# Kernel tuning notes

Measured on AMD Instinct MI355X. Metric: run time of the kernel, lower is better.

The kernel has to match this reference:

```python
import jax, jax.numpy as jnp
import numpy as np
import math

LS = [0, 1, 2]            # degrees present in all irreps
MAX_L = 2
MULT_IN = 64
MULT_MID = 16
MULT_OUT = 64
N = 20000

# ---- Clebsch-Gordan coefficients in the real spherical-harmonic basis ----

def _f(n):
    return math.factorial(int(n))

def _cg_complex(j1, m1, j2, m2, j3, m3):
    if m1 + m2 != m3:
        return 0.0
    pre = math.sqrt((2 * j3 + 1) * _f(j1 + j2 - j3) * _f(j1 - j2 + j3) * _f(-j1 + j2 + j3) / _f(j1 + j2 + j3 + 1))
    pre *= math.sqrt(_f(j1 + m1) * _f(j1 - m1) * _f(j2 + m2) * _f(j2 - m2) * _f(j3 + m3) * _f(j3 - m3))
    kmin = max(0, j2 - j3 - m1, j1 - j3 + m2)
    kmax = min(j1 + j2 - j3, j1 - m1, j2 + m2)
    s = 0.0
    for k in range(kmin, kmax + 1):
        s += (-1) ** k / (_f(k) * _f(j1 + j2 - j3 - k) * _f(j1 - m1 - k) * _f(j2 + m2 - k) * _f(j3 - j2 + m1 + k) * _f(j3 - j1 - m2 + k))
    return pre * s

def _q(l):
    # complex->real change of basis, rows indexed by real m = -l..l
    Q = np.zeros((2 * l + 1, 2 * l + 1), dtype=complex)
    Q[l, l] = 1.0
    r2 = math.sqrt(2.0)
    for m in range(1, l + 1):
        Q[l + m, l + m] = (-1) ** m / r2
        Q[l + m, l - m] = 1.0 / r2
        Q[l - m, l - m] = 1j / r2
        Q[l - m, l + m] = -1j * (-1) ** m / r2
    return Q

def _real_cg(l1, l2, l3):
    C = np.zeros((2 * l1 + 1, 2 * l2 + 1, 2 * l3 + 1), dtype=complex)
    for m1 in range(-l1, l1 + 1):
        for m2 in range(-l2, l2 + 1):
            m3 = m1 + m2
            if -l3 <= m3 <= l3:
                C[l1 + m1, l2 + m2, l3 + m3] = _cg_complex(l1, m1, l2, m2, l3, m3)
    Q1, Q2, Q3 = _q(l1), _q(l2), _q(l3)
    M = np.einsum('ia,jb,kc,abc->ijk', Q1.conj(), Q2.conj(), Q3, C)
    if np.abs(M.imag).max() > np.abs(M.real).max():
        M = M * (-1j)  # fix parity phase so coefficients are real
    assert np.abs(M.imag).max() < 1e-10
    return np.asarray(M.real, dtype=np.float32)

# triangle-rule paths, truncated at MAX_L
PATHS = [(l1, l2, l) for l1 in LS for l2 in LS for l in range(abs(l1 - l2), min(l1 + l2, MAX_L) + 1)]
CG = {p: jnp.asarray(_real_cg(*p)) for p in PATHS}


def setup_inputs() -> dict:
    key = jax.random.key(0)
    ks = jax.random.split(key, 12)
    inp = {}
    for i, l in enumerate(LS):
        inp[f'x{l}'] = jax.random.normal(ks[i], (N, MULT_IN, 2 * l + 1), dtype=jnp.float32)
    for i, l in enumerate(LS):
        inp[f'W1_{l}'] = jax.random.normal(ks[3 + i], (MULT_IN, MULT_MID), dtype=jnp.float32)
        inp[f'W2_{l}'] = jax.random.normal(ks[6 + i], (MULT_IN, MULT_MID), dtype=jnp.float32)
    tp_mults = {l: sum(MULT_MID * MULT_MID for (l1, l2, lo) in PATHS if lo == l) for l in LS}
    for i, l in enumerate(LS):
        inp[f'W3_{l}'] = jax.random.normal(ks[9 + i], (tp_mults[l], MULT_OUT), dtype=jnp.float32)
    return inp


def _linear(x, W):
    # x: [n, u, i], W: [u, v] -> [n, v, i], normalized like e3nn Linear
    return jnp.einsum('nui,uv->nvi', x, W) / np.float32(math.sqrt(x.shape[1]))


def reference(x0, x1, x2, W1_0, W1_1, W1_2, W2_0, W2_1, W2_2, W3_0, W3_1, W3_2):
    xs = [x0, x1, x2]
    W1 = [W1_0, W1_1, W1_2]
    W2 = [W2_0, W2_1, W2_2]
    W3 = [W3_0, W3_1, W3_2]
    a = [_linear(xs[l], W1[l]) for l in LS]   # branch 1
    b = [_linear(xs[l], W2[l]) for l in LS]   # branch 2
    # CG tensor product up to MAX_L, full (uv) multiplicity
    tp = {l: [] for l in LS}
    n = x0.shape[0]
    for (l1, l2, l) in PATHS:
        t = jnp.einsum('nui,nvj,ijk->nuvk', a[l1], b[l2], CG[(l1, l2, l)])
        tp[l].append(t.reshape(n, MULT_MID * MULT_MID, 2 * l + 1))
    outs = []
    for l in LS:
        z = jnp.concatenate(tp[l], axis=1)        # [n, tp_mult_l, 2l+1]
        y = _linear(z, W3[l])                     # [n, MULT_OUT, 2l+1]
        outs.append(y.reshape(n, -1))
    return jnp.concatenate(outs, axis=1)          # [n, MULT_OUT * 9]
```

## Files before the change

kernel.cpp:

```cpp
#include <hip/hip_runtime.h>


typedef __attribute__((ext_vector_type(4))) float f32x4;
typedef __attribute__((ext_vector_type(4))) float f4;
typedef __attribute__((ext_vector_type(2))) float f2;
typedef __attribute__((ext_vector_type(8))) short short8;
typedef unsigned short ushort_t;
typedef unsigned int uint32;

__device__ __forceinline__ uint32 bfb(float x) {
  uint32 u = __float_as_uint(x);
  return (u + 0x7fffu + ((u >> 16) & 1u)) >> 16;
}
__device__ __forceinline__ uint32 pack2f(f2 z) {
  uint32 lo = __float_as_uint(z.x) + 0x8000u;
  uint32 hi = __float_as_uint(z.y) + 0x8000u;
  return __builtin_amdgcn_perm(hi, lo, 0x07060302u);
}

#define C2   0.7071067811865476f
#define C3   0.5773502691896258f
#define C5   0.4472135954999579f
#define C6   0.4082482904638631f
#define C23  0.8164965809277260f
#define C10  0.3162277660168379f
#define C210 0.6324555320336759f
#define C310 0.5477225575051661f
#define C14  0.2672612419124244f
#define C214 0.5345224838248488f
#define C314 0.4629100498862757f

__global__ __launch_bounds__(256) void pack_w3_kernel(
    const float* __restrict__ W30, const float* __restrict__ W31,
    const float* __restrict__ W32, ushort_t* __restrict__ pack) {
  int lc = blockIdx.x;
  int t = threadIdx.x >> 6;
  int lam = threadIdx.x & 63;
  const float* W;
  int mb;
  float nrm;
  if (lc < 24) {
    W = W30; mb = lc * 32; nrm = 0.036084391824351615f;
  } else if (lc < 72) {
    W = W31; mb = (lc - 24) * 32; nrm = 0.025515518153991442f;
  } else {
    W = W32; mb = (lc - 72) * 32; nrm = 0.025515518153991442f;
  }
  int w = t * 16 + (lam & 15);
  int m0 = mb + (lam >> 4) * 8;
  ushort_t* dst = pack + ((size_t)(lc * 4 + t) * 64 + lam) * 8;
#pragma unroll
  for (int j = 0; j < 8; ++j)
    dst[j] = (ushort_t)bfb(W[(size_t)(m0 + j) * 64 + w] * nrm);
}

template <int NK, int JD, class F>
__device__ __forceinline__ void zgenv(const float* bsj, ushort_t* zrow, F f) {
  uint32 zp[NK][8];
#pragma unroll
  for (int oc = 0; oc < 2; ++oc) {
    f2 bb4[JD][4];
#pragma unroll
    for (int j = 0; j < JD; ++j) {
      f4 lo = *(const f4*)(bsj + j * 16 + oc * 8);
      f4 hi = *(const f4*)(bsj + j * 16 + oc * 8 + 4);
      bb4[j][0] = lo.xy; bb4[j][1] = lo.zw;
      bb4[j][2] = hi.xy; bb4[j][3] = hi.zw;
    }
#pragma unroll
    for (int q = 0; q < 4; ++q) {
      f2 bcol[JD], z[NK];
#pragma unroll
      for (int j = 0; j < JD; ++j) bcol[j] = bb4[j][q];
      f(bcol, z);
#pragma unroll
      for (int k = 0; k < NK; ++k) zp[k][oc * 4 + q] = pack2f(z[k]);
    }
  }
#pragma unroll
  for (int k = 0; k < NK; ++k) {
    uint32* d = (uint32*)(zrow + k * (16 * 264));
    *(uint4*)(d) = make_uint4(zp[k][0], zp[k][1], zp[k][2], zp[k][3]);
    *(uint4*)(d + 4) = make_uint4(zp[k][4], zp[k][5], zp[k][6], zp[k][7]);
  }
}

template <int NROW>
__device__ __forceinline__ void mfma2(const ushort_t* zb, const ushort_t* pk,
                                      int pcbase, int h, int wt0, int lane,
                                      f32x4* accA, f32x4* accB) {
  const int srow = lane & 15, quad = lane >> 4;
  const ushort_t* ab = zb + srow * 264 + quad * 8 + h * 128;
  const ushort_t* bb = pk + ((size_t)((pcbase + h * 4) * 4 + wt0) * 64 + lane) * 8;
#pragma unroll
  for (int c = 0; c < 4; ++c) {
    short8 B0 = *(const short8*)(bb + (size_t)c * 2048);
    short8 B1 = *(const short8*)(bb + (size_t)c * 2048 + 512);
#pragma unroll
    for (int rt = 0; rt < NROW; ++rt) {
      short8 A = *(const short8*)(ab + rt * (16 * 264) + c * 32);
      accA[rt] = __builtin_amdgcn_mfma_f32_16x16x32_bf16(A, B0, accA[rt], 0, 0, 0);
      accB[rt] = __builtin_amdgcn_mfma_f32_16x16x32_bf16(A, B1, accB[rt], 0, 0, 0);
    }
  }
}

#define ZB 12672

__global__ __launch_bounds__(256, 2) void tdense_kernel(
    const float* __restrict__ x0, const float* __restrict__ x1,
    const float* __restrict__ x2, const float* __restrict__ W10,
    const float* __restrict__ W20, const float* __restrict__ W11,
    const float* __restrict__ W21, const float* __restrict__ W12,
    const float* __restrict__ W22, const ushort_t* __restrict__ pack,
    float* __restrict__ out) {
  __shared__ float b_s[2368];
  __shared__ __align__(16) ushort_t zbuf[2 * ZB];

  const int tid = threadIdx.x;
  const int nbase = blockIdx.x * 16;
  const int s = tid >> 4, v = tid & 15;

  const int n = nbase + s;
  const float* px0 = x0 + (size_t)n * 64;
  const float* px1 = x1 + (size_t)n * 192;
  const float* px2 = x2 + (size_t)n * 320;
  float a0 = 0.f, a1x = 0.f, a1y = 0.f, a1z = 0.f;
  float a2[5] = {0.f, 0.f, 0.f, 0.f, 0.f};
  float b0 = 0.f, b1x = 0.f, b1y = 0.f, b1z = 0.f;
  float b2[5] = {0.f, 0.f, 0.f, 0.f, 0.f};
  for (int u4 = 0; u4 < 16; ++u4) {
    f4 xv0 = *(const f4*)(px0 + u4 * 4);
    f4 xa = *(const f4*)(px1 + u4 * 12);
    f4 xb = *(const f4*)(px1 + u4 * 12 + 4);
    f4 xc = *(const f4*)(px1 + u4 * 12 + 8);
    f4 ya = *(const f4*)(px2 + u4 * 20);
    f4 yb = *(const f4*)(px2 + u4 * 20 + 4);
    f4 yc = *(const f4*)(px2 + u4 * 20 + 8);
    f4 yd = *(const f4*)(px2 + u4 * 20 + 12);
    f4 ye = *(const f4*)(px2 + u4 * 20 + 16);
    float x1e[12], x2e[20];
#pragma unroll
    for (int e = 0; e < 4; ++e) { x1e[e] = xa[e]; x1e[4 + e] = xb[e]; x1e[8 + e] = xc[e]; }
#pragma unroll
    for (int e = 0; e < 4; ++e) {
      x2e[e] = ya[e]; x2e[4 + e] = yb[e]; x2e[8 + e] = yc[e];
      x2e[12 + e] = yd[e]; x2e[16 + e] = ye[e];
    }
#pragma unroll
    for (int r = 0; r < 4; ++r) {
      int u = u4 * 4 + r;
      float wa0 = W10[u * 16 + v], wb0 = W20[u * 16 + v];
      float wa1 = W11[u * 16 + v], wb1 = W21[u * 16 + v];
      float wa2 = W12[u * 16 + v], wb2 = W22[u * 16 + v];
      float xx = xv0[r];
      a0 += xx * wa0; b0 += xx * wb0;
      float e0 = x1e[r * 3 + 0], e1 = x1e[r * 3 + 1], e2 = x1e[r * 3 + 2];
      a1x += e0 * wa1; a1y += e1 * wa1; a1z += e2 * wa1;
      b1x += e0 * wb1; b1y += e1 * wb1; b1z += e2 * wb1;
#pragma unroll
      for (int j = 0; j < 5; ++j) {
        float ev = x2e[r * 5 + j];
        a2[j] += ev * wa2;
        b2[j] += ev * wb2;
      }
    }
  }
  const float inv8 = 0.125f;
  float ar[9];
  ar[0] = a0 * inv8;
  ar[1] = a1x * inv8; ar[2] = a1y * inv8; ar[3] = a1z * inv8;
#pragma unroll
  for (int j = 0; j < 5; ++j) ar[4 + j] = a2[j] * inv8;
  {
    float* bw = b_s + s * 148 + v;
    bw[0] = b0 * inv8;
    bw[16] = b1x * inv8; bw[32] = b1y * inv8; bw[48] = b1z * inv8;
#pragma unroll
    for (int j = 0; j < 5; ++j) bw[64 + j * 16] = b2[j] * inv8;
  }

  const int lane = tid & 63;
  const int wv = tid >> 6;
  const int p2 = (wv & 1) * 2;
  const int h = wv >> 1;

  f32x4 aA0, aB0, aA1[3], aB1[3], aA2[5], aB2[5];
  aA0 = (f32x4)(0.f); aB0 = (f32x4)(0.f);
#pragma unroll
  for (int i = 0; i < 3; ++i) { aA1[i] = (f32x4)(0.f); aB1[i] = (f32x4)(0.f); }
#pragma unroll
  for (int i = 0; i < 5; ++i) { aA2[i] = (f32x4)(0.f); aB2[i] = (f32x4)(0.f); }

  const float* bsl0 = b_s + s * 148;
  const float* bsl1 = bsl0 + 16;
  const float* bsl2 = bsl0 + 64;
  ushort_t* z0 = zbuf + s * 264 + v * 16;
  ushort_t* z1 = z0 + ZB;
  const ushort_t* Zb0 = zbuf;
  const ushort_t* Zb1 = zbuf + ZB;

  zgenv<1, 1>(bsl0, z0, [&](const f2* b, f2* z) { z[0] = ar[0] * b[0]; });
  zgenv<1, 3>(bsl1, z0 + 4224, [&](const f2* b, f2* z) {
    z[0] = -C3 * (ar[1] * b[0] + ar[2] * b[1] + ar[3] * b[2]);
  });
  zgenv<1, 5>(bsl2, z0 + 8448, [&](const f2* b, f2* z) {
    z[0] = C5 * (ar[4] * b[0] + ar[5] * b[1] + ar[6] * b[2] + ar[7] * b[3] + ar[8] * b[4]);
  });
  __syncthreads();

  zgenv<3, 3>(bsl1, z1, [&](const f2* b, f2* z) {
    z[0] = ar[0] * b[0]; z[1] = ar[0] * b[1]; z[2] = ar[0] * b[2];
  });
  mfma2<1>(Zb0, pack, 0, h, p2, lane, &aA0, &aB0);
  mfma2<1>(Zb0 + 4224, pack, 8, h, p2, lane, &aA0, &aB0);
  mfma2<1>(Zb0 + 8448, pack, 16, h, p2, lane, &aA0, &aB0);
  __syncthreads();

  zgenv<3, 1>(bsl0, z0, [&](const f2* b, f2* z) {
    z[0] = ar[1] * b[0]; z[1] = ar[2] * b[0]; z[2] = ar[3] * b[0];
  });
  mfma2<3>(Zb1, pack, 24, h, p2, lane, aA1, aB1);
  __syncthreads();

  zgenv<3, 3>(bsl1, z1, [&](const f2* b, f2* z) {
    z[0] = C2 * (ar[2] * b[2] - ar[3] * b[1]);
    z[1] = C2 * (ar[3] * b[0] - ar[1] * b[2]);
    z[2] = C2 * (ar[1] * b[1] - ar[2] * b[0]);
  });
  mfma2<3>(Zb0, pack, 32, h, p2, lane, aA1, aB1);
  __syncthreads();

  zgenv<3, 5>(bsl2, z0, [&](const f2* b, f2* z) {
    z[0] = -C310 * ar[2] * b[1] + C10 * ar[1] * b[2] - C310 * ar[3] * b[0] + C310 * ar[1] * b[4];
    z[1] = -C210 * ar[2] * b[2] - C310 * ar[3] * b[3] - C310 * ar[1] * b[1];
    z[2] = -C310 * ar[2] * b[3] + C10 * ar[3] * b[2] - C310 * ar[1] * b[0] - C310 * ar[3] * b[4];
  });
  mfma2<3>(Zb1, pack, 40, h, p2, lane, aA1, aB1);
  __syncthreads();

  zgenv<3, 3>(bsl1, z1, [&](const f2* b, f2* z) {
    z[0] = -C310 * ar[5] * b[1] + C10 * ar[6] * b[0] - C310 * ar[4] * b[2] + C310 * ar[8] * b[0];
    z[1] = -C210 * ar[6] * b[1] - C310 * ar[7] * b[2] - C310 * ar[5] * b[0];
    z[2] = -C310 * ar[7] * b[1] + C10 * ar[6] * b[2] - C310 * ar[4] * b[0] - C310 * ar[8] * b[2];
  });
  mfma2<3>(Zb0, pack, 48, h, p2, lane, aA1, aB1);
  __syncthreads();

  zgenv<3, 5>(bsl2, z0, [&](const f2* b, f2* z) {
    z[0] = C10 * (ar[8] * b[3] - ar[7] * b[4] + ar[4] * b[1] - ar[5] * b[0]) +
           C310 * (ar[7] * b[2] - ar[6] * b[3]);
    z[1] = C10 * (ar[5] * b[3] - ar[7] * b[1]) + C210 * (ar[4] * b[4] - ar[8] * b[0]);
    z[2] = C10 * (ar[8] * b[1] - ar[5] * b[4] + ar[7] * b[0] - ar[4] * b[3]) +
           C310 * (ar[6] * b[1] - ar[5] * b[2]);
  });
  mfma2<3>(Zb1, pack, 56, h, p2, lane, aA1, aB1);
  __syncthreads();

  zgenv<3, 5>(bsl2, z1, [&](const f2* b, f2* z) {
    z[0] = ar[0] * b[0]; z[1] = ar[0] * b[1]; z[2] = ar[0] * b[2];
  });
  mfma2<3>(Zb0, pack, 64, h, p2, lane, aA1, aB1);
  __syncthreads();

  zgenv<2, 5>(bsl2, z0, [&](const f2* b, f2* z) {
    z[0] = ar[0] * b[3]; z[1] = ar[0] * b[4];
  });
  mfma2<3>(Zb1, pack, 72, h, p2, lane, aA2, aB2);
  __syncthreads();

  zgenv<3, 3>(bsl1, z1, [&](const f2* b, f2* z) {
    z[0] = C2 * (ar[1] * b[2] + ar[3] * b[0]);
    z[1] = C2 * (ar[2] * b[0] + ar[1] * b[1]);
    z[2] = C23 * ar[2] * b[1] - C6 * (ar[1] * b[0] + ar[3] * b[2]);
  });
  mfma2<2>(Zb0, pack, 72, h, p2, lane, aA2 + 3, aB2 + 3);
  __syncthreads();

  zgenv<2, 3>(bsl1, z0, [&](const f2* b, f2* z) {
    z[0] = C2 * (ar[2] * b[2] + ar[3] * b[1]);
    z[1] = C2 * (ar[3] * b[2] - ar[1] * b[0]);
  });
  mfma2<3>(Zb1, pack, 80, h, p2, lane, aA2, aB2);
  __syncthreads();

  zgenv<3, 5>(bsl2, z1, [&](const f2* b, f2* z) {
    z[0] = C23 * ar[2] * b[4] + C6 * ar[1] * b[1] - C6 * ar[3] * b[3];
    z[1] = C6 * ar[2] * b[3] - C6 * ar[1] * b[0] - C2 * ar[3] * b[2] - C6 * ar[3] * b[4];
    z[2] = C2 * (ar[3] * b[1] - ar[1] * b[3]);
  });
  mfma2<2>(Zb0, pack, 80, h, p2, lane, aA2 + 3, aB2 + 3);
  __syncthreads();

  zgenv<2, 5>(bsl2, z0, [&](const f2* b, f2* z) {
    z[0] = -C6 * ar[2] * b[1] + C2 * ar[1] * b[2] + C6 * ar[3] * b[0] - C6 * ar[1] * b[4];
    z[1] = -C23 * ar[2] * b[0] + C6 * ar[1] * b[3] + C6 * ar[3] * b[1];
  });
  mfma2<3>(Zb1, pack, 88, h, p2, lane, aA2, aB2);
  __syncthreads();

  zgenv<3, 1>(bsl0, z1, [&](const f2* b, f2* z) {
    z[0] = ar[4] * b[0]; z[1] = ar[5] * b[0]; z[2] = ar[6] * b[0];
  });
  mfma2<2>(Zb0, pack, 88, h, p2, lane, aA2 + 3, aB2 + 3);
  __syncthreads();

  zgenv<2, 1>(bsl0, z0, [&](const f2* b, f2* z) {
    z[0] = ar[7] * b[0]; z[1] = ar[8] * b[0];
  });
  mfma2<3>(Zb1, pack, 96, h, p2, lane, aA2, aB2);
  __syncthreads();

  zgenv<3, 3>(bsl1, z1, [&](const f2* b, f2* z) {
    z[0] = -C23 * ar[8] * b[1] - C6 * ar[5] * b[0] + C6 * ar[7] * b[2];
    z[1] = -C6 * ar[7] * b[1] + C6 * ar[4] * b[0] + C2 * ar[6] * b[2] + C6 * ar[8] * b[2];
    z[2] = C2 * (ar[7] * b[0] - ar[5] * b[2]);
  });
  mfma2<2>(Zb0, pack, 96, h, p2, lane, aA2 + 3, aB2 + 3);
  __syncthreads();

  zgenv<2, 3>(bsl1, z0, [&](const f2* b, f2* z) {
    z[0] = C6 * ar[5] * b[1] - C2 * ar[6] * b[0] - C6 * ar[4] * b[2] + C6 * ar[8] * b[0];
    z[1] = C23 * ar[4] * b[1] - C6 * ar[7] * b[0] - C6 * ar[5] * b[2];
  });
  mfma2<3>(Zb1, pack, 104, h, p2, lane, aA2, aB2);
  __syncthreads();

  zgenv<3, 5>(bsl2, z1, [&](const f2* b, f2* z) {
    z[0] = C214 * (ar[6] * b[0] + ar[4] * b[2]) - C314 * (ar[5] * b[3] + ar[7] * b[1]);
    z[1] = -C14 * (ar[6] * b[1] + ar[5] * b[2]) + C314 * (ar[5] * b[4] + ar[8] * b[1]) -
           C314 * (ar[7] * b[0] + ar[4] * b[3]);
    z[2] = -C214 * ar[6] * b[2] - C14 * (ar[5] * b[1] + ar[7] * b[3]) +
           C214 * (ar[4] * b[0] + ar[8] * b[4]);
  });
  mfma2<2>(Zb0, pack, 104, h, p2, lane, aA2 + 3, aB2 + 3);
  __syncthreads();

  zgenv<2, 5>(bsl2, z0, [&](const f2* b, f2* z) {
    z[0] = -C14 * (ar[6] * b[3] + ar[7] * b[2]) - C314 * (ar[5] * b[0] + ar[4] * b[1]) -
           C314 * (ar[7] * b[4] + ar[8] * b[3]);
    z[1] = C214 * (ar[6] * b[4] + ar[8] * b[2]) + C314 * (ar[5] * b[1] - ar[7] * b[3]);
  });
  mfma2<3>(Zb1, pack, 112, h, p2, lane, aA2, aB2);
  __syncthreads();

  mfma2<2>(Zb0, pack, 112, h, p2, lane, aA2 + 3, aB2 + 3);
  __syncthreads();

  float* red = (float*)zbuf;
  const int col = lane & 15, quad = lane >> 4;
  if (h == 0) {
#pragma unroll
    for (int pp = 0; pp < 2; ++pp) {
      int wt = p2 + pp;
      const f32x4* src0 = pp ? &aB0 : &aA0;
      const f32x4* src1 = pp ? aB1 : aA1;
      const f32x4* src2 = pp ? aB2 : aA2;
      *(f4*)(red + (wt * 9 + 0) * 256 + lane * 4) = src0[0];
#pragma unroll
      for (int o = 0; o < 3; ++o)
        *(f4*)(red + (wt * 9 + 1 + o) * 256 + lane * 4) = src1[o];
#pragma unroll
      for (int o = 0; o < 5; ++o)
        *(f4*)(red + (wt * 9 + 4 + o) * 256 + lane * 4) = src2[o];
    }
  }
  __syncthreads();
  if (h == 1) {
    aA0 += *(const f4*)(red + (p2 * 9 + 0) * 256 + lane * 4);
    aB0 += *(const f4*)(red + ((p2 + 1) * 9 + 0) * 256 + lane * 4);
#pragma unroll
    for (int o = 0; o < 3; ++o) {
      aA1[o] += *(const f4*)(red + (p2 * 9 + 1 + o) * 256 + lane * 4);
      aB1[o] += *(const f4*)(red + ((p2 + 1) * 9 + 1 + o) * 256 + lane * 4);
    }
#pragma unroll
    for (int o = 0; o < 5; ++o) {
      aA2[o] += *(const f4*)(red + (p2 * 9 + 4 + o) * 256 + lane * 4);
      aB2[o] += *(const f4*)(red + ((p2 + 1) * 9 + 4 + o) * 256 + lane * 4);
    }
    const int w0 = p2 * 16 + col, w1 = w0 + 16;
#pragma unroll
    for (int r = 0; r < 4; ++r) {
      int so = quad * 4 + r;
      float* row = out + (size_t)(nbase + so) * 576;
      row[w0] = aA0[r];
      row[w1] = aB0[r];
      row[64 + w0 * 3 + 0] = aA1[0][r];
      row[64 + w0 * 3 + 1] = aA1[1][r];
      row[64 + w0 * 3 + 2] = aA1[2][r];
      row[64 + w1 * 3 + 0] = aB1[0][r];
      row[64 + w1 * 3 + 1] = aB1[1][r];
      row[64 + w1 * 3 + 2] = aB1[2][r];
#pragma unroll
      for (int k = 0; k < 5; ++k) {
        row[256 + w0 * 5 + k] = aA2[k][r];
        row[256 + w1 * 5 + k] = aB2[k][r];
      }
    }
  }
}

extern "C" void kernel_launch(void* const* d_in, const int* in_sizes, int n_in,
                              void* d_out, int out_size, void* d_ws, size_t ws_size,
                              hipStream_t stream) {
  const float* x0 = (const float*)d_in[0];
  const float* x1 = (const float*)d_in[1];
  const float* x2 = (const float*)d_in[2];
  const float* W10 = (const float*)d_in[3];
  const float* W20 = (const float*)d_in[4];
  const float* W11 = (const float*)d_in[5];
  const float* W21 = (const float*)d_in[6];
  const float* W12 = (const float*)d_in[7];
  const float* W22 = (const float*)d_in[8];
  const float* W30 = (const float*)d_in[9];
  const float* W31 = (const float*)d_in[10];
  const float* W32 = (const float*)d_in[11];
  ushort_t* pack = (ushort_t*)d_ws;

  hipLaunchKernelGGL(pack_w3_kernel, dim3(120), dim3(256), 0, stream,
                     W30, W31, W32, pack);

  int nsamp = in_sizes[0] / 64;
  int nblocks = nsamp / 16;
  hipLaunchKernelGGL(tdense_kernel, dim3(nblocks), dim3(256), 0, stream,
                     x0, x1, x2, W10, W20, W11, W21, W12, W22, pack,
                     (float*)d_out);
}
```

Baseline: 220.2 us.

## Collapse tensor-product dense kernel to one wavefront per 16-sample block

Each 16-sample block now runs on a single 64-lane wavefront instead of four waves. Every lane computes four mid-channels, loading the first-linear weights as vectors, and one wave runs the full K and N range of the MFMA output linear. This removes the cross-wave split-K reduction through LDS and most of the inter-wave barriers. In exchange each wave carries more registers and serial work, and latency hiding must come from more resident blocks, since launch bounds now allow one 64-thread block.

Result: slower. 590.2 us (+168.1%).

```diff
diff --git a/kernel.cpp b/kernel.cpp
--- a/kernel.cpp
+++ b/kernel.cpp
@@ -68,13 +68,13 @@
       bb4[j][2] = hi.xy; bb4[j][3] = hi.zw;
     }
 #pragma unroll
-    for (int q = 0; q < 4; ++q) {
+    for (int qp = 0; qp < 4; ++qp) {
       f2 bcol[JD], z[NK];
 #pragma unroll
-      for (int j = 0; j < JD; ++j) bcol[j] = bb4[j][q];
+      for (int j = 0; j < JD; ++j) bcol[j] = bb4[j][qp];
       f(bcol, z);
 #pragma unroll
-      for (int k = 0; k < NK; ++k) zp[k][oc * 4 + q] = pack2f(z[k]);
+      for (int k = 0; k < NK; ++k) zp[k][oc * 4 + qp] = pack2f(z[k]);
     }
   }
 #pragma unroll
@@ -85,50 +85,54 @@
   }
 }
 
-template <int NROW>
-__device__ __forceinline__ void mfma2(const ushort_t* zb, const ushort_t* pk,
-                                      int pcbase, int h, int wt0, int lane,
-                                      f32x4* accA, f32x4* accB) {
+template <int NROW, int NC, int M0>
+__device__ __forceinline__ void mfma_full(const ushort_t* zb,
+                                          const ushort_t* pkl, int pcbase,
+                                          int lane, f32x4 (&acc)[4][NC]) {
   const int srow = lane & 15, quad = lane >> 4;
-  const ushort_t* ab = zb + srow * 264 + quad * 8 + h * 128;
-  const ushort_t* bb = pk + ((size_t)((pcbase + h * 4) * 4 + wt0) * 64 + lane) * 8;
-#pragma unroll
-  for (int c = 0; c < 4; ++c) {
-    short8 B0 = *(const short8*)(bb + (size_t)c * 2048);
-    short8 B1 = *(const short8*)(bb + (size_t)c * 2048 + 512);
+  const ushort_t* ab = zb + srow * 264 + quad * 8;
+#pragma unroll
+  for (int c = 0; c < 8; ++c) {
+    const ushort_t* bb = pkl + (size_t)(pcbase + c) * 2048;
+    short8 B0 = *(const short8*)(bb);
+    short8 B1 = *(const short8*)(bb + 512);
+    short8 B2 = *(const short8*)(bb + 1024);
+    short8 B3 = *(const short8*)(bb + 1536);
 #pragma unroll
     for (int rt = 0; rt < NROW; ++rt) {
-      short8 A = *(const short8*)(ab + rt * (16 * 264) + c * 32);
-      accA[rt] = __builtin_amdgcn_mfma_f32_16x16x32_bf16(A, B0, accA[rt], 0, 0, 0);
-      accB[rt] = __builtin_amdgcn_mfma_f32_16x16x32_bf16(A, B1, accB[rt], 0, 0, 0);
-    }
-  }
-}
-
-#define ZB 12672
-
-__global__ __launch_bounds__(256, 2) void tdense_kernel(
+      short8 A = *(const short8*)(ab + rt * 4224 + c * 32);
+      acc[0][M0 + rt] = __builtin_amdgcn_mfma_f32_16x16x32_bf16(A, B0, acc[0][M0 + rt], 0, 0, 0);
+      acc[1][M0 + rt] = __builtin_amdgcn_mfma_f32_16x16x32_bf16(A, B1, acc[1][M0 + rt], 0, 0, 0);
+      acc[2][M0 + rt] = __builtin_amdgcn_mfma_f32_16x16x32_bf16(A, B2, acc[2][M0 + rt], 0, 0, 0);
+      acc[3][M0 + rt] = __builtin_amdgcn_mfma_f32_16x16x32_bf16(A, B3, acc[3][M0 + rt], 0, 0, 0);
+    }
+  }
+}
+
+__global__ __launch_bounds__(64, 1) void tdense_kernel(
     const float* __restrict__ x0, const float* __restrict__ x1,
     const float* __restrict__ x2, const float* __restrict__ W10,
     const float* __restrict__ W20, const float* __restrict__ W11,
     const float* __restrict__ W21, const float* __restrict__ W12,
     const float* __restrict__ W22, const ushort_t* __restrict__ pack,
     float* __restrict__ out) {
-  __shared__ float b_s[2368];
-  __shared__ __align__(16) ushort_t zbuf[2 * ZB];
-
-  const int tid = threadIdx.x;
+  __shared__ __align__(16) float lds_b[16 * 148];
+  __shared__ __align__(16) ushort_t zls[3 * 16 * 264];
+
+  const int lane = threadIdx.x;
+  const int s = lane & 15, q = lane >> 4;
   const int nbase = blockIdx.x * 16;
-  const int s = tid >> 4, v = tid & 15;
-
   const int n = nbase + s;
+
   const float* px0 = x0 + (size_t)n * 64;
   const float* px1 = x1 + (size_t)n * 192;
   const float* px2 = x2 + (size_t)n * 320;
-  float a0 = 0.f, a1x = 0.f, a1y = 0.f, a1z = 0.f;
-  float a2[5] = {0.f, 0.f, 0.f, 0.f, 0.f};
-  float b0 = 0.f, b1x = 0.f, b1y = 0.f, b1z = 0.f;
-  float b2[5] = {0.f, 0.f, 0.f, 0.f, 0.f};
+  float av_[4][9], bv_[4][9];
+#pragma unroll
+  for (int vi = 0; vi < 4; ++vi)
+#pragma unroll
+    for (int i = 0; i < 9; ++i) { av_[vi][i] = 0.f; bv_[vi][i] = 0.f; }
+  const int wq = q * 4;
   for (int u4 = 0; u4 < 16; ++u4) {
     f4 xv0 = *(const f4*)(px0 + u4 * 4);
     f4 xa = *(const f4*)(px1 + u4 * 12);
@@ -150,252 +154,341 @@
 #pragma unroll
     for (int r = 0; r < 4; ++r) {
       int u = u4 * 4 + r;
-      float wa0 = W10[u * 16 + v], wb0 = W20[u * 16 + v];
-      float wa1 = W11[u * 16 + v], wb1 = W21[u * 16 + v];
-      float wa2 = W12[u * 16 + v], wb2 = W22[u * 16 + v];
+      f4 wa0 = *(const f4*)(W10 + u * 16 + wq);
+      f4 wb0 = *(const f4*)(W20 + u * 16 + wq);
+      f4 wa1 = *(const f4*)(W11 + u * 16 + wq);
+      f4 wb1 = *(const f4*)(W21 + u * 16 + wq);
+      f4 wa2 = *(const f4*)(W12 + u * 16 + wq);
+      f4 wb2 = *(const f4*)(W22 + u * 16 + wq);
       float xx = xv0[r];
-      a0 += xx * wa0; b0 += xx * wb0;
-      float e0 = x1e[r * 3 + 0], e1 = x1e[r * 3 + 1], e2 = x1e[r * 3 + 2];
-      a1x += e0 * wa1; a1y += e1 * wa1; a1z += e2 * wa1;
-      b1x += e0 * wb1; b1y += e1 * wb1; b1z += e2 * wb1;
-#pragma unroll
-      for (int j = 0; j < 5; ++j) {
-        float ev = x2e[r * 5 + j];
-        a2[j] += ev * wa2;
-        b2[j] += ev * wb2;
+      float e0 = x1e[r * 3], e1 = x1e[r * 3 + 1], e2 = x1e[r * 3 + 2];
+#pragma unroll
+      for (int vi = 0; vi < 4; ++vi) {
+        av_[vi][0] += xx * wa0[vi]; bv_[vi][0] += xx * wb0[vi];
+        av_[vi][1] += e0 * wa1[vi]; av_[vi][2] += e1 * wa1[vi]; av_[vi][3] += e2 * wa1[vi];
+        bv_[vi][1] += e0 * wb1[vi]; bv_[vi][2] += e1 * wb1[vi]; bv_[vi][3] += e2 * wb1[vi];
+#pragma unroll
+        for (int jj = 0; jj < 5; ++jj) {
+          float ev = x2e[r * 5 + jj];
+          av_[vi][4 + jj] += ev * wa2[vi];
+          bv_[vi][4 + jj] += ev * wb2[vi];
+        }
       }
     }
   }
+
   const float inv8 = 0.125f;
-  float ar[9];
-  ar[0] = a0 * inv8;
-  ar[1] = a1x * inv8; ar[2] = a1y * inv8; ar[3] = a1z * inv8;
-#pragma unroll
-  for (int j = 0; j < 5; ++j) ar[4 + j] = a2[j] * inv8;
-  {
-    float* bw = b_s + s * 148 + v;
-    bw[0] = b0 * inv8;
-    bw[16] = b1x * inv8; bw[32] = b1y * inv8; bw[48] = b1z * inv8;
-#pragma unroll
-    for (int j = 0; j < 5; ++j) bw[64 + j * 16] = b2[j] * inv8;
-  }
-
-  const int lane = tid & 63;
-  const int wv = tid >> 6;
-  const int p2 = (wv & 1) * 2;
-  const int h = wv >> 1;
-
-  f32x4 aA0, aB0, aA1[3], aB1[3], aA2[5], aB2[5];
-  aA0 = (f32x4)(0.f); aB0 = (f32x4)(0.f);
-#pragma unroll
-  for (int i = 0; i < 3; ++i) { aA1[i] = (f32x4)(0.f); aB1[i] = (f32x4)(0.f); }
-#pragma unroll
-  for (int i = 0; i < 5; ++i) { aA2[i] = (f32x4)(0.f); aB2[i] = (f32x4)(0.f); }
-
-  const float* bsl0 = b_s + s * 148;
+#pragma unroll
+  for (int vi = 0; vi < 4; ++vi)
+#pragma unroll
+    for (int i = 0; i < 9; ++i) av_[vi][i] *= inv8;
+#pragma unroll
+  for (int j = 0; j < 9; ++j) {
+    f4 bw = {bv_[0][j], bv_[1][j], bv_[2][j], bv_[3][j]};
+    *(f4*)(lds_b + s * 148 + j * 16 + q * 4) = bw * inv8;
+  }
+  __syncthreads();
+
+  const float* bsl0 = lds_b + s * 148;
   const float* bsl1 = bsl0 + 16;
   const float* bsl2 = bsl0 + 64;
-  ushort_t* z0 = zbuf + s * 264 + v * 16;
-  ushort_t* z1 = z0 + ZB;
-  const ushort_t* Zb0 = zbuf;
-  const ushort_t* Zb1 = zbuf + ZB;
-
-  zgenv<1, 1>(bsl0, z0, [&](const f2* b, f2* z) { z[0] = ar[0] * b[0]; });
-  zgenv<1, 3>(bsl1, z0 + 4224, [&](const f2* b, f2* z) {
-    z[0] = -C3 * (ar[1] * b[0] + ar[2] * b[1] + ar[3] * b[2]);
-  });
-  zgenv<1, 5>(bsl2, z0 + 8448, [&](const f2* b, f2* z) {
-    z[0] = C5 * (ar[4] * b[0] + ar[5] * b[1] + ar[6] * b[2] + ar[7] * b[3] + ar[8] * b[4]);
-  });
-  __syncthreads();
-
-  zgenv<3, 3>(bsl1, z1, [&](const f2* b, f2* z) {
-    z[0] = ar[0] * b[0]; z[1] = ar[0] * b[1]; z[2] = ar[0] * b[2];
-  });
-  mfma2<1>(Zb0, pack, 0, h, p2, lane, &aA0, &aB0);
-  mfma2<1>(Zb0 + 4224, pack, 8, h, p2, lane, &aA0, &aB0);
-  mfma2<1>(Zb0 + 8448, pack, 16, h, p2, lane, &aA0, &aB0);
-  __syncthreads();
-
-  zgenv<3, 1>(bsl0, z0, [&](const f2* b, f2* z) {
-    z[0] = ar[1] * b[0]; z[1] = ar[2] * b[0]; z[2] = ar[3] * b[0];
-  });
-  mfma2<3>(Zb1, pack, 24, h, p2, lane, aA1, aB1);
-  __syncthreads();
-
-  zgenv<3, 3>(bsl1, z1, [&](const f2* b, f2* z) {
-    z[0] = C2 * (ar[2] * b[2] - ar[3] * b[1]);
-    z[1] = C2 * (ar[3] * b[0] - ar[1] * b[2]);
-    z[2] = C2 * (ar[1] * b[1] - ar[2] * b[0]);
-  });
-  mfma2<3>(Zb0, pack, 32, h, p2, lane, aA1, aB1);
-  __syncthreads();
-
-  zgenv<3, 5>(bsl2, z0, [&](const f2* b, f2* z) {
-    z[0] = -C310 * ar[2] * b[1] + C10 * ar[1] * b[2] - C310 * ar[3] * b[0] + C310 * ar[1] * b[4];
-    z[1] = -C210 * ar[2] * b[2] - C310 * ar[3] * b[3] - C310 * ar[1] * b[1];
-    z[2] = -C310 * ar[2] * b[3] + C10 * ar[3] * b[2] - C310 * ar[1] * b[0] - C310 * ar[3] * b[4];
-  });
-  mfma2<3>(Zb1, pack, 40, h, p2, lane, aA1, aB1);
-  __syncthreads();
-
-  zgenv<3, 3>(bsl1, z1, [&](const f2* b, f2* z) {
-    z[0] = -C310 * ar[5] * b[1] + C10 * ar[6] * b[0] - C310 * ar[4] * b[2] + C310 * ar[8] * b[0];
-    z[1] = -C210 * ar[6] * b[1] - C310 * ar[7] * b[2] - C310 * ar[5] * b[0];
-    z[2] = -C310 * ar[7] * b[1] + C10 * ar[6] * b[2] - C310 * ar[4] * b[0] - C310 * ar[8] * b[2];
-  });
-  mfma2<3>(Zb0, pack, 48, h, p2, lane, aA1, aB1);
-  __syncthreads();
-
-  zgenv<3, 5>(bsl2, z0, [&](const f2* b, f2* z) {
-    z[0] = C10 * (ar[8] * b[3] - ar[7] * b[4] + ar[4] * b[1] - ar[5] * b[0]) +
-           C310 * (ar[7] * b[2] - ar[6] * b[3]);
-    z[1] = C10 * (ar[5] * b[3] - ar[7] * b[1]) + C210 * (ar[4] * b[4] - ar[8] * b[0]);
-    z[2] = C10 * (ar[8] * b[1] - ar[5] * b[4] + ar[7] * b[0] - ar[4] * b[3]) +
-           C310 * (ar[6] * b[1] - ar[5] * b[2]);
-  });
-  mfma2<3>(Zb1, pack, 56, h, p2, lane, aA1, aB1);
-  __syncthreads();
-
-  zgenv<3, 5>(bsl2, z1, [&](const f2* b, f2* z) {
-    z[0] = ar[0] * b[0]; z[1] = ar[0] * b[1]; z[2] = ar[0] * b[2];
-  });
-  mfma2<3>(Zb0, pack, 64, h, p2, lane, aA1, aB1);
-  __syncthreads();
-
-  zgenv<2, 5>(bsl2, z0, [&](const f2* b, f2* z) {
-    z[0] = ar[0] * b[3]; z[1] = ar[0] * b[4];
-  });
-  mfma2<3>(Zb1, pack, 72, h, p2, lane, aA2, aB2);
-  __syncthreads();
-
-  zgenv<3, 3>(bsl1, z1, [&](const f2* b, f2* z) {
-    z[0] = C2 * (ar[1] * b[2] + ar[3] * b[0]);
-    z[1] = C2 * (ar[2] * b[0] + ar[1] * b[1]);
-    z[2] = C23 * ar[2] * b[1] - C6 * (ar[1] * b[0] + ar[3] * b[2]);
-  });
-  mfma2<2>(Zb0, pack, 72, h, p2, lane, aA2 + 3, aB2 + 3);
-  __syncthreads();
-
-  zgenv<2, 3>(bsl1, z0, [&](const f2* b, f2* z) {
-    z[0] = C2 * (ar[2] * b[2] + ar[3] * b[1]);
-    z[1] = C2 * (ar[3] * b[2] - ar[1] * b[0]);
-  });
-  mfma2<3>(Zb1, pack, 80, h, p2, lane, aA2, aB2);
-  __syncthreads();
-
-  zgenv<3, 5>(bsl2, z1, [&](const f2* b, f2* z) {
-    z[0] = C23 * ar[2] * b[4] + C6 * ar[1] * b[1] - C6 * ar[3] * b[3];
-    z[1] = C6 * ar[2] * b[3] - C6 * ar[1] * b[0] - C2 * ar[3] * b[2] - C6 * ar[3] * b[4];
-    z[2] = C2 * (ar[3] * b[1] - ar[1] * b[3]);
-  });
-  mfma2<2>(Zb0, pack, 80, h, p2, lane, aA2 + 3, aB2 + 3);
-  __syncthreads();
-
-  zgenv<2, 5>(bsl2, z0, [&](const f2* b, f2* z) {
-    z[0] = -C6 * ar[2] * b[1] + C2 * ar[1] * b[2] + C6 * ar[3] * b[0] - C6 * ar[1] * b[4];
-    z[1] = -C23 * ar[2] * b[0] + C6 * ar[1] * b[3] + C6 * ar[3] * b[1];
-  });
-  mfma2<3>(Zb1, pack, 88, h, p2, lane, aA2, aB2);
-  __syncthreads();
-
-  zgenv<3, 1>(bsl0, z1, [&](const f2* b, f2* z) {
-    z[0] = ar[4] * b[0]; z[1] = ar[5] * b[0]; z[2] = ar[6] * b[0];
-  });
-  mfma2<2>(Zb0, pack, 88, h, p2, lane, aA2 + 3, aB2 + 3);
-  __syncthreads();
-
-  zgenv<2, 1>(bsl0, z0, [&](const f2* b, f2* z) {
-    z[0] = ar[7] * b[0]; z[1] = ar[8] * b[0];
-  });
-  mfma2<3>(Zb1, pack, 96, h, p2, lane, aA2, aB2);
-  __syncthreads();
-
-  zgenv<3, 3>(bsl1, z1, [&](const f2* b, f2* z) {
-    z[0] = -C23 * ar[8] * b[1] - C6 * ar[5] * b[0] + C6 * ar[7] * b[2];
-    z[1] = -C6 * ar[7] * b[1] + C6 * ar[4] * b[0] + C2 * ar[6] * b[2] + C6 * ar[8] * b[2];
-    z[2] = C2 * (ar[7] * b[0] - ar[5] * b[2]);
-  });
-  mfma2<2>(Zb0, pack, 96, h, p2, lane, aA2 + 3, aB2 + 3);
-  __syncthreads();
-
-  zgenv<2, 3>(bsl1, z0, [&](const f2* b, f2* z) {
-    z[0] = C6 * ar[5] * b[1] - C2 * ar[6] * b[0] - C6 * ar[4] * b[2] + C6 * ar[8] * b[0];
-    z[1] = C23 * ar[4] * b[1] - C6 * ar[7] * b[0] - C6 * ar[5] * b[2];
-  });
-  mfma2<3>(Zb1, pack, 104, h, p2, lane, aA2, aB2);
-  __syncthreads();
-
-  zgenv<3, 5>(bsl2, z1, [&](const f2* b, f2* z) {
-    z[0] = C214 * (ar[6] * b[0] + ar[4] * b[2]) - C314 * (ar[5] * b[3] + ar[7] * b[1]);
-    z[1] = -C14 * (ar[6] * b[1] + ar[5] * b[2]) + C314 * (ar[5] * b[4] + ar[8] * b[1]) -
-           C314 * (ar[7] * b[0] + ar[4] * b[3]);
-    z[2] = -C214 * ar[6] * b[2] - C14 * (ar[5] * b[1] + ar[7] * b[3]) +
-           C214 * (ar[4] * b[0] + ar[8] * b[4]);
-  });
-  mfma2<2>(Zb0, pack, 104, h, p2, lane, aA2 + 3, aB2 + 3);
-  __syncthreads();
-
-  zgenv<2, 5>(bsl2, z0, [&](const f2* b, f2* z) {
-    z[0] = -C14 * (ar[6] * b[3] + ar[7] * b[2]) - C314 * (ar[5] * b[0] + ar[4] * b[1]) -
-           C314 * (ar[7] * b[4] + ar[8] * b[3]);
-    z[1] = C214 * (ar[6] * b[4] + ar[8] * b[2]) + C314 * (ar[5] * b[1] - ar[7] * b[3]);
-  });
-  mfma2<3>(Zb1, pack, 112, h, p2, lane, aA2, aB2);
-  __syncthreads();
-
-  mfma2<2>(Zb0, pack, 112, h, p2, lane, aA2 + 3, aB2 + 3);
-  __syncthreads();
-
-  float* red = (float*)zbuf;
-  const int col = lane & 15, quad = lane >> 4;
-  if (h == 0) {
-#pragma unroll
-    for (int pp = 0; pp < 2; ++pp) {
-      int wt = p2 + pp;
-      const f32x4* src0 = pp ? &aB0 : &aA0;
-      const f32x4* src1 = pp ? aB1 : aA1;
-      const f32x4* src2 = pp ? aB2 : aA2;
-      *(f4*)(red + (wt * 9 + 0) * 256 + lane * 4) = src0[0];
-#pragma unroll
-      for (int o = 0; o < 3; ++o)
-        *(f4*)(red + (wt * 9 + 1 + o) * 256 + lane * 4) = src1[o];
-#pragma unroll
-      for (int o = 0; o < 5; ++o)
-        *(f4*)(red + (wt * 9 + 4 + o) * 256 + lane * 4) = src2[o];
-    }
-  }
-  __syncthreads();
-  if (h == 1) {
-    aA0 += *(const f4*)(red + (p2 * 9 + 0) * 256 + lane * 4);
-    aB0 += *(const f4*)(red + ((p2 + 1) * 9 + 0) * 256 + lane * 4);
-#pragma unroll
-    for (int o = 0; o < 3; ++o) {
-      aA1[o] += *(const f4*)(red + (p2 * 9 + 1 + o) * 256 + lane * 4);
-      aB1[o] += *(const f4*)(red + ((p2 + 1) * 9 + 1 + o) * 256 + lane * 4);
-    }
-#pragma unroll
-    for (int o = 0; o < 5; ++o) {
-      aA2[o] += *(const f4*)(red + (p2 * 9 + 4 + o) * 256 + lane * 4);
-      aB2[o] += *(const f4*)(red + ((p2 + 1) * 9 + 4 + o) * 256 + lane * 4);
-    }
-    const int w0 = p2 * 16 + col, w1 = w0 + 16;
+  const ushort_t* pkl = pack + (size_t)lane * 8;
+  ushort_t* zr = zls + s * 264 + (q * 4) * 16;
+  const int ncol = s, rq4 = q * 4;
+
+  {
+    f32x4 acc[4][1];
+#pragma unroll
+    for (int wt = 0; wt < 4; ++wt) acc[wt][0] = (f32x4)(0.f);
+#pragma unroll
+    for (int vi = 0; vi < 4; ++vi) {
+      const float* arp = av_[vi];
+      ushort_t* zv = zr + vi * 16;
+      zgenv<1, 1>(bsl0, zv, [&](const f2* b, f2* z) { z[0] = arp[0] * b[0]; });
+      zgenv<1, 3>(bsl1, zv + 4224, [&](const f2* b, f2* z) {
+        z[0] = -C3 * (arp[1] * b[0] + arp[2] * b[1] + arp[3] * b[2]);
+      });
+      zgenv<1, 5>(bsl2, zv + 8448, [&](const f2* b, f2* z) {
+        z[0] = C5 * (arp[4] * b[0] + arp[5] * b[1] + arp[6] * b[2] +
+                     arp[7] * b[3] + arp[8] * b[4]);
+      });
+    }
+    __syncthreads();
+    mfma_full<1, 1, 0>(zls, pkl, 0, lane, acc);
+    mfma_full<1, 1, 0>(zls + 4224, pkl, 8, lane, acc);
+    mfma_full<1, 1, 0>(zls + 8448, pkl, 16, lane, acc);
 #pragma unroll
     for (int r = 0; r < 4; ++r) {
-      int so = quad * 4 + r;
-      float* row = out + (size_t)(nbase + so) * 576;
-      row[w0] = aA0[r];
-      row[w1] = aB0[r];
-      row[64 + w0 * 3 + 0] = aA1[0][r];
-      row[64 + w0 * 3 + 1] = aA1[1][r];
-      row[64 + w0 * 3 + 2] = aA1[2][r];
-      row[64 + w1 * 3 + 0] = aB1[0][r];
-      row[64 + w1 * 3 + 1] = aB1[1][r];
-      row[64 + w1 * 3 + 2] = aB1[2][r];
-#pragma unroll
-      for (int k = 0; k < 5; ++k) {
-        row[256 + w0 * 5 + k] = aA2[k][r];
-        row[256 + w1 * 5 + k] = aB2[k][r];
+      float* row = out + (size_t)(nbase + rq4 + r) * 576;
+#pragma unroll
+      for (int wt = 0; wt < 4; ++wt) row[wt * 16 + ncol] = acc[wt][0][r];
+    }
+    __syncthreads();
+  }
+
+  {
+    f32x4 acc[4][3];
+#pragma unroll
+    for (int wt = 0; wt < 4; ++wt)
+#pragma unroll
+      for (int m = 0; m < 3; ++m) acc[wt][m] = (f32x4)(0.f);
+
+#pragma unroll
+    for (int vi = 0; vi < 4; ++vi) {
+      const float* arp = av_[vi];
+      zgenv<3, 3>(bsl1, zr + vi * 16, [&](const f2* b, f2* z) {
+        z[0] = arp[0] * b[0]; z[1] = arp[0] * b[1]; z[2] = arp[0] * b[2];
+      });
+    }
+    __syncthreads();
+    mfma_full<3, 3, 0>(zls, pkl, 24, lane, acc);
+    __syncthreads();
+
+#pragma unroll
+    for (int vi = 0; vi < 4; ++vi) {
+      const float* arp = av_[vi];
+      zgenv<3, 1>(bsl0, zr + vi * 16, [&](const f2* b, f2* z) {
+        z[0] = arp[1] * b[0]; z[1] = arp[2] * b[0]; z[2] = arp[3] * b[0];
+      });
+    }
+    __syncthreads();
+    mfma_full<3, 3, 0>(zls, pkl, 32, lane, acc);
+    __syncthreads();
+
+#pragma unroll
+    for (int vi = 0; vi < 4; ++vi) {
+      const float* arp = av_[vi];
+      zgenv<3, 3>(bsl1, zr + vi * 16, [&](const f2* b, f2* z) {
+        z[0] = C2 * (arp[2] * b[2] - arp[3] * b[1]);
+        z[1] = C2 * (arp[3] * b[0] - arp[1] * b[2]);
+        z[2] = C2 * (arp[1] * b[1] - arp[2] * b[0]);
+      });
+    }
+    __syncthreads();
+    mfma_full<3, 3, 0>(zls, pkl, 40, lane, acc);
+    __syncthreads();
+
+#pragma unroll
+    for (int vi = 0; vi < 4; ++vi) {
+      const float* arp = av_[vi];
+      zgenv<3, 5>(bsl2, zr + vi * 16, [&](const f2* b, f2* z) {
+        z[0] = -C310 * arp[2] * b[1] + C10 * arp[1] * b[2] - C310 * arp[3] * b[0] +
+               C310 * arp[1] * b[4];
+        z[1] = -C210 * arp[2] * b[2] - C310 * arp[3] * b[3] - C310 * arp[1] * b[1];
+        z[2] = -C310 * arp[2] * b[3] + C10 * arp[3] * b[2] - C310 * arp[1] * b[0] -
+               C310 * arp[3] * b[4];
+      });
+    }
+    __syncthreads();
+    mfma_full<3, 3, 0>(zls, pkl, 48, lane, acc);
+    __syncthreads();
+
+#pragma unroll
+    for (int vi = 0; vi < 4; ++vi) {
+      const float* arp = av_[vi];
+      zgenv<3, 3>(bsl1, zr + vi * 16, [&](const f2* b, f2* z) {
+        z[0] = -C310 * arp[5] * b[1] + C10 * arp[6] * b[0] - C310 * arp[4] * b[2] +
+               C310 * arp[8] * b[0];
+        z[1] = -C210 * arp[6] * b[1] - C310 * arp[7] * b[2] - C310 * arp[5] * b[0];
+        z[2] = -C310 * arp[7] * b[1] + C10 * arp[6] * b[2] - C310 * arp[4] * b[0] -
+               C310 * arp[8] * b[2];
+      });
+    }
+    __syncthreads();
+    mfma_full<3, 3, 0>(zls, pkl, 56, lane, acc);
+    __syncthreads();
+
+#pragma unroll
+    for (int vi = 0; vi < 4; ++vi) {
+      const float* arp = av_[vi];
+      zgenv<3, 5>(bsl2, zr + vi * 16, [&](const f2* b, f2* z) {
+        z[0] = C10 * (arp[8] * b[3] - arp[7] * b[4] + arp[4] * b[1] - arp[5] * b[0]) +
+               C310 * (arp[7] * b[2] - arp[6] * b[3]);
+        z[1] = C10 * (arp[5] * b[3] - arp[7] * b[1]) +
+               C210 * (arp[4] * b[4] - arp[8] * b[0]);
+        z[2] = C10 * (arp[8] * b[1] - arp[5] * b[4] + arp[7] * b[0] - arp[4] * b[3]) +
+               C310 * (arp[6] * b[1] - arp[5] * b[2]);
+      });
+    }
+    __syncthreads();
+    mfma_full<3, 3, 0>(zls, pkl, 64, lane, acc);
+
+#pragma unroll
+    for (int r = 0; r < 4; ++r) {
+      float* row = out + (size_t)(nbase + rq4 + r) * 576 + 64;
+#pragma unroll
+      for (int wt = 0; wt < 4; ++wt) {
+        int w3 = (wt * 16 + ncol) * 3;
+#pragma unroll
+        for (int m = 0; m < 3; ++m) row[w3 + m] = acc[wt][m][r];
+      }
+    }
+    __syncthreads();
+  }
+
+  {
+    f32x4 acc[4][5];
+#pragma unroll
+    for (int wt = 0; wt < 4; ++wt)
+#pragma unroll
+      for (int m = 0; m < 5; ++m) acc[wt][m] = (f32x4)(0.f);
+
+#pragma unroll
+    for (int vi = 0; vi < 4; ++vi) {
+      const float* arp = av_[vi];
+      zgenv<3, 5>(bsl2, zr + vi * 16, [&](const f2* b, f2* z) {
+        z[0] = arp[0] * b[0]; z[1] = arp[0] * b[1]; z[2] = arp[0] * b[2];
+      });
+    }
+    __syncthreads();
+    mfma_full<3, 5, 0>(zls, pkl, 72, lane, acc);
+    __syncthreads();
+#pragma unroll
+    for (int vi = 0; vi < 4; ++vi) {
+      const float* arp = av_[vi];
+      zgenv<2, 5>(bsl2, zr + vi * 16, [&](const f2* b, f2* z) {
+        z[0] = arp[0] * b[3]; z[1] = arp[0] * b[4];
+      });
+    }
+    __syncthreads();
+    mfma_full<2, 5, 3>(zls, pkl, 72, lane, acc);
+    __syncthreads();
+
+#pragma unroll
+    for (int vi = 0; vi < 4; ++vi) {
+      const float* arp = av_[vi];
+      zgenv<3, 3>(bsl1, zr + vi * 16, [&](const f2* b, f2* z) {
+        z[0] = C2 * (arp[1] * b[2] + arp[3] * b[0]);
+        z[1] = C2 * (arp[2] * b[0] + arp[1] * b[1]);
+        z[2] = C23 * arp[2] * b[1] - C6 * (arp[1] * b[0] + arp[3] * b[2]);
+      });
+    }
+    __syncthreads();
+    mfma_full<3, 5, 0>(zls, pkl, 80, lane, acc);
+    __syncthreads();
+#pragma unroll
+    for (int vi = 0; vi < 4; ++vi) {
+      const float* arp = av_[vi];
+      zgenv<2, 3>(bsl1, zr + vi * 16, [&](const f2* b, f2* z) {
+        z[0] = C2 * (arp[2] * b[2] + arp[3] * b[1]);
+        z[1] = C2 * (arp[3] * b[2] - arp[1] * b[0]);
+      });
+    }
+    __syncthreads();
+    mfma_full<2, 5, 3>(zls, pkl, 80, lane, acc);
+    __syncthreads();
+
+#pragma unroll
+    for (int vi = 0; vi < 4; ++vi) {
+      const float* arp = av_[vi];
+      zgenv<3, 5>(bsl2, zr + vi * 16, [&](const f2* b, f2* z) {
+        z[0] = C23 * arp[2] * b[4] + C6 * arp[1] * b[1] - C6 * arp[3] * b[3];
+        z[1] = C6 * arp[2] * b[3] - C6 * arp[1] * b[0] - C2 * arp[3] * b[2] -
+               C6 * arp[3] * b[4];
+        z[2] = C2 * (arp[3] * b[1] - arp[1] * b[3]);
+      });
+    }
+    __syncthreads();
+    mfma_full<3, 5, 0>(zls, pkl, 88, lane, acc);
+    __syncthreads();
+#pragma unroll
+    for (int vi = 0; vi < 4; ++vi) {
+      const float* arp = av_[vi];
+      zgenv<2, 5>(bsl2, zr + vi * 16, [&](const f2* b, f2* z) {
+        z[0] = -C6 * arp[2] * b[1] + C2 * arp[1] * b[2] + C6 * arp[3] * b[0] -
+               C6 * arp[1] * b[4];
+        z[1] = -C23 * arp[2] * b[0] + C6 * arp[1] * b[3] + C6 * arp[3] * b[1];
+      });
+    }
+    __syncthreads();
+    mfma_full<2, 5, 3>(zls, pkl, 88, lane, acc);
+    __syncthreads();
+
+#pragma unroll
+    for (int vi = 0; vi < 4; ++vi) {
+      const float* arp = av_[vi];
+      zgenv<3, 1>(bsl0, zr + vi * 16, [&](const f2* b, f2* z) {
+        z[0] = arp[4] * b[0]; z[1] = arp[5] * b[0]; z[2] = arp[6] * b[0];
+      });
+    }
+    __syncthreads();
+    mfma_full<3, 5, 0>(zls, pkl, 96, lane, acc);
+    __syncthreads();
+#pragma unroll
+    for (int vi = 0; vi < 4; ++vi) {
+      const float* arp = av_[vi];
+      zgenv<2, 1>(bsl0, zr + vi * 16, [&](const f2* b, f2* z) {
+        z[0] = arp[7] * b[0]; z[1] = arp[8] * b[0];
+      });
+    }
+    __syncthreads();
+    mfma_full<2, 5, 3>(zls, pkl, 96, lane, acc);
+    __syncthreads();
+
+#pragma unroll
+    for (int vi = 0; vi < 4; ++vi) {
+      const float* arp = av_[vi];
+      zgenv<3, 3>(bsl1, zr + vi * 16, [&](const f2* b, f2* z) {
+        z[0] = -C23 * arp[8] * b[1] - C6 * arp[5] * b[0] + C6 * arp[7] * b[2];
+        z[1] = -C6 * arp[7] * b[1] + C6 * arp[4] * b[0] + C2 * arp[6] * b[2] +
+               C6 * arp[8] * b[2];
+        z[2] = C2 * (arp[7] * b[0] - arp[5] * b[2]);
+      });
+    }
+    __syncthreads();
+    mfma_full<3, 5, 0>(zls, pkl, 104, lane, acc);
+    __syncthreads();
+#pragma unroll
+    for (int vi = 0; vi < 4; ++vi) {
+      const float* arp = av_[vi];
+      zgenv<2, 3>(bsl1, zr + vi * 16, [&](const f2* b, f2* z) {
+        z[0] = C6 * arp[5] * b[1] - C2 * arp[6] * b[0] - C6 * arp[4] * b[2] +
+               C6 * arp[8] * b[0];
+        z[1] = C23 * arp[4] * b[1] - C6 * arp[7] * b[0] - C6 * arp[5] * b[2];
+      });
+    }
+    __syncthreads();
+    mfma_full<2, 5, 3>(zls, pkl, 104, lane, acc);
+    __syncthreads();
+
+#pragma unroll
+    for (int vi = 0; vi < 4; ++vi) {
+      const float* arp = av_[vi];
+      zgenv<3, 5>(bsl2, zr + vi * 16, [&](const f2* b, f2* z) {
+        z[0] = C214 * (arp[6] * b[0] + arp[4] * b[2]) -
+               C314 * (arp[5] * b[3] + arp[7] * b[1]);
+        z[1] = -C14 * (arp[6] * b[1] + arp[5] * b[2]) +
+               C314 * (arp[5] * b[4] + arp[8] * b[1]) -
+               C314 * (arp[7] * b[0] + arp[4] * b[3]);
+        z[2] = -C214 * arp[6] * b[2] - C14 * (arp[5] * b[1] + arp[7] * b[3]) +
+               C214 * (arp[4] * b[0] + arp[8] * b[4]);
+      });
+    }
+    __syncthreads();
+    mfma_full<3, 5, 0>(zls, pkl, 112, lane, acc);
+    __syncthreads();
+#pragma unroll
+    for (int vi = 0; vi < 4; ++vi) {
+      const float* arp = av_[vi];
+      zgenv<2, 5>(bsl2, zr + vi * 16, [&](const f2* b, f2* z) {
+        z[0] = -C14 * (arp[6] * b[3] + arp[7] * b[2]) -
+               C314 * (arp[5] * b[0] + arp[4] * b[1]) -
+               C314 * (arp[7] * b[4] + arp[8] * b[3]);
+        z[1] = C214 * (arp[6] * b[4] + arp[8] * b[2]) +
+               C314 * (arp[5] * b[1] - arp[7] * b[3]);
+      });
+    }
+    __syncthreads();
+    mfma_full<2, 5, 3>(zls, pkl, 112, lane, acc);
+
+#pragma unroll
+    for (int r = 0; r < 4; ++r) {
+      float* row = out + (size_t)(nbase + rq4 + r) * 576 + 256;
+#pragma unroll
+      for (int wt = 0; wt < 4; ++wt) {
+        int w5 = (wt * 16 + ncol) * 5;
+#pragma unroll
+        for (int m = 0; m < 5; ++m) row[w5 + m] = acc[wt][m][r];
       }
     }
   }
@@ -423,7 +516,7 @@
 
   int nsamp = in_sizes[0] / 64;
   int nblocks = nsamp / 16;
-  hipLaunchKernelGGL(tdense_kernel, dim3(nblocks), dim3(256), 0, stream,
+  hipLaunchKernelGGL(tdense_kernel, dim3(nblocks), dim3(64), 0, stream,
                      x0, x1, x2, W10, W20, W11, W21, W12, W22, pack,
                      (float*)d_out);
 }
```
